# Kernel optimization log

Measured on AMD Instinct MI355X. Metric: run time of the kernel, lower is better.

## Reference

```python
import jax, jax.numpy as jnp
import numpy as np
from jax import lax

B, H, W, CIN = 4, 64, 64, 1024
CMID = 512
NA = 9  # 3 sizes * 3 ratios
PRE_NMS, POST_NMS, IOU_THR = 6000, 300, 0.7  # eval-mode caps (training=False)


def setup_inputs() -> dict:
    key = jax.random.key(0)
    ks = jax.random.split(key, 4)
    feats = jax.random.normal(ks[0], (B, H, W, CIN), jnp.float32)
    # anchors: normalized ccwh (cx, cy, w, h) on a stride-16 grid of a 1024px image
    stride, img = 16.0, 1024.0
    cx = (jnp.arange(W, dtype=jnp.float32) + 0.5) * stride / img
    cy = (jnp.arange(H, dtype=jnp.float32) + 0.5) * stride / img
    sizes = jnp.array([64.0, 128.0, 256.0])
    ratios = jnp.array([0.5, 1.0, 2.0])
    ws = (sizes[:, None] * jnp.sqrt(ratios)[None, :]).reshape(-1) / img  # [9]
    hs = (sizes[:, None] / jnp.sqrt(ratios)[None, :]).reshape(-1) / img  # [9]
    cyg, cxg = jnp.meshgrid(cy, cx, indexing='ij')  # [H,W]
    ancs = jnp.stack([
        jnp.broadcast_to(cxg[:, :, None], (H, W, NA)),
        jnp.broadcast_to(cyg[:, :, None], (H, W, NA)),
        jnp.broadcast_to(ws[None, None, :], (H, W, NA)),
        jnp.broadcast_to(hs[None, None, :], (H, W, NA)),
    ], axis=-1)
    ancs = jnp.broadcast_to(ancs[None], (B, H, W, NA, 4)).astype(jnp.float32)
    ancs_valid = jnp.ones((B, H, W, NA), jnp.float32)
    w_bneck = jax.random.normal(ks[1], (CIN, CMID), jnp.float32) * 0.01
    b_bneck = jnp.zeros((CMID,), jnp.float32)
    w_cls = jax.random.normal(ks[2], (CMID, NA), jnp.float32) * 0.01
    b_cls = jnp.zeros((NA,), jnp.float32)
    w_reg = jax.random.normal(ks[3], (CMID, NA * 4), jnp.float32) * 0.01
    b_reg = jnp.zeros((NA * 4,), jnp.float32)
    return dict(feats=feats, ancs=ancs, ancs_valid=ancs_valid,
                w_bneck=w_bneck, b_bneck=b_bneck, w_cls=w_cls, b_cls=b_cls,
                w_reg=w_reg, b_reg=b_reg)


def _nms(boxes, max_out, thr):
    # boxes [N,4] xyxy, sorted by score descending. Greedy NMS via lax.scan.
    x1, y1, x2, y2 = boxes[:, 0], boxes[:, 1], boxes[:, 2], boxes[:, 3]
    areas = (x2 - x1) * (y2 - y1)

    def step(valid, _):
        idx = jnp.argmax(valid)  # first still-valid box = highest score
        has = valid[idx]
        b = boxes[idx]
        a = areas[idx]
        iw = jnp.maximum(jnp.minimum(b[2], x2) - jnp.maximum(b[0], x1), 0.0)
        ih = jnp.maximum(jnp.minimum(b[3], y2) - jnp.maximum(b[1], y1), 0.0)
        inter = iw * ih
        union = a + areas - inter
        iou = jnp.where(union > 0, inter / union, 0.0)
        keep = valid & (iou <= thr)
        keep = keep.at[idx].set(False)
        return jnp.where(has, keep, valid), jnp.where(has, idx, -1)

    _, sel = lax.scan(step, jnp.ones(boxes.shape[0], bool), None, length=max_out)
    return sel  # [max_out] selected indices, -1 = no more boxes


def _forward(feats, ancs, w_bneck, b_bneck, w_cls, b_cls, w_reg, b_reg):
    h = jax.nn.relu(jnp.einsum('bhwc,cm->bhwm', feats, w_bneck) + b_bneck)
    cls_pred = jax.nn.sigmoid(jnp.einsum('bhwm,mo->bhwo', h, w_cls) + b_cls)
    reg_pred = (jnp.einsum('bhwm,mo->bhwo', h, w_reg) + b_reg).reshape(B, H, W, NA, 4)
    cls_f = cls_pred.reshape(-1)
    reg_f = reg_pred.reshape(-1, 4)
    anc_f = ancs.reshape(-1, 4)
    # apply_offsets in ccwh: cx += tx*w, cy += ty*h, w *= exp(tw), h *= exp(th)
    cx = anc_f[:, 0] + reg_f[:, 0] * anc_f[:, 2]
    cy = anc_f[:, 1] + reg_f[:, 1] * anc_f[:, 3]
    ww = anc_f[:, 2] * jnp.exp(reg_f[:, 2])
    hh = anc_f[:, 3] * jnp.exp(reg_f[:, 3])
    # ccwh -> xyxy, clip to [0,1]
    boxes = jnp.stack([cx - ww / 2, cy - hh / 2, cx + ww / 2, cy + hh / 2], axis=-1)
    boxes = jnp.clip(boxes, 0.0, 1.0)
    order = jnp.argsort(-cls_f)[:PRE_NMS]
    boxes = boxes[order]
    sel = _nms(boxes, POST_NMS, IOU_THR)
    # pad unselected slots with zeros (TF returns a variable-length tensor)
    proposals = jnp.where(sel[:, None] >= 0, boxes[jnp.clip(sel, 0)], 0.0)
    return cls_pred, reg_pred, proposals


def reference(feats, ancs, ancs_valid, w_bneck, b_bneck, w_cls, b_cls, w_reg, b_reg):
    # ancs_valid is reshaped but never used in the original extract_proposals
    return _forward(feats, ancs, w_bneck, b_bneck, w_cls, b_cls, w_reg, b_reg)
```

## Files before the change

### kernel.cpp

```cpp
#include <hip/hip_runtime.h>
#include <cstdint>
#include <cstddef>

#define P_TOT    16384
#define CIN      1024
#define CMID     512
#define NA       9
#define NANC     147456
#define PRE_NMS  6000
#define POST_NMS 300
#define IOU_THR  0.7f
#define NWORDS   94
#define NHCOPY   8

#define CLS_OFF  0
#define REG_OFF  147456
#define PROP_OFF 737280

#define WS_H        0u
#define WS_MASK     0u
#define WS_HISTN    33554432u
#define WS_BOXES    36700160u
#define WS_HIST     39059456u
#define WS_WCOMB    39059456u
#define WS_META     39321600u
#define WS_COLL     39321856u
#define WS_SBOX     39387392u
#define CAP_COLL    8192

__device__ __forceinline__ int imin(int a, int b) { return a < b ? a : b; }

__device__ __forceinline__ void gld_lds16f(const float* g, float* l) {
    __builtin_amdgcn_global_load_lds(
        (const __attribute__((address_space(1))) void*)g,
        (__attribute__((address_space(3))) void*)l,
        16, 0, 0);
}

__global__ __launch_bounds__(256)
__attribute__((amdgpu_waves_per_eu(1, 2)))
void gemm1_kernel(
    const float* __restrict__ A, const float* __restrict__ Bw,
    const float* __restrict__ bias, float* __restrict__ C)
{
    __shared__ float As[2][32][132];
    __shared__ float Bs[2][32][128];

    const int t  = threadIdx.x;
    const int m0 = blockIdx.x * 128;
    const int n0 = blockIdx.y * 128;
    const int tx = t & 15;
    const int ty = t >> 4;

    const int ar0 = t >> 1;
    const int ac0 = (t & 1) * 16;

    const float* asrc = A + (size_t)(m0 + ar0) * CIN + ac0;
    const float* bsrc = Bw + (size_t)(t >> 5) * CMID + n0 + (t & 31) * 4;
    float* bflat = &Bs[0][0][0];

    float4 c0a{0,0,0,0}, c0b{0,0,0,0}, c1a{0,0,0,0}, c1b{0,0,0,0};
    float4 c2a{0,0,0,0}, c2b{0,0,0,0}, c3a{0,0,0,0}, c3b{0,0,0,0};
    float4 c4a{0,0,0,0}, c4b{0,0,0,0}, c5a{0,0,0,0}, c5b{0,0,0,0};
    float4 c6a{0,0,0,0}, c6b{0,0,0,0}, c7a{0,0,0,0}, c7b{0,0,0,0};

#define ASTAGE(buf, v0, v1, v2, v3) { \
    As[buf][ac0 +  0][ar0] = v0.x; As[buf][ac0 +  1][ar0] = v0.y; \
    As[buf][ac0 +  2][ar0] = v0.z; As[buf][ac0 +  3][ar0] = v0.w; \
    As[buf][ac0 +  4][ar0] = v1.x; As[buf][ac0 +  5][ar0] = v1.y; \
    As[buf][ac0 +  6][ar0] = v1.z; As[buf][ac0 +  7][ar0] = v1.w; \
    As[buf][ac0 +  8][ar0] = v2.x; As[buf][ac0 +  9][ar0] = v2.y; \
    As[buf][ac0 + 10][ar0] = v2.z; As[buf][ac0 + 11][ar0] = v2.w; \
    As[buf][ac0 + 12][ar0] = v3.x; As[buf][ac0 + 13][ar0] = v3.y; \
    As[buf][ac0 + 14][ar0] = v3.z; As[buf][ac0 + 15][ar0] = v3.w; }

    {
        gld_lds16f(bsrc,                      bflat +    0 + t * 4);
        gld_lds16f(bsrc + (size_t) 8 * CMID,  bflat + 1024 + t * 4);
        gld_lds16f(bsrc + (size_t)16 * CMID,  bflat + 2048 + t * 4);
        gld_lds16f(bsrc + (size_t)24 * CMID,  bflat + 3072 + t * 4);
        float4 av0 = *(const float4*)(asrc + 0);
        float4 av1 = *(const float4*)(asrc + 4);
        float4 av2 = *(const float4*)(asrc + 8);
        float4 av3 = *(const float4*)(asrc + 12);
        ASTAGE(0, av0, av1, av2, av3)
    }
    __syncthreads();

#define FMA4(acc, s, b) { acc.x += (s)*(b).x; acc.y += (s)*(b).y; \
                          acc.z += (s)*(b).z; acc.w += (s)*(b).w; }

    for (int kt = 0; kt < 32; ++kt) {
        const int cur = kt & 1, nxt = cur ^ 1;
        float4 av0, av1, av2, av3;
        if (kt < 31) {
            const int k0 = (kt + 1) * 32;
            float* bd = bflat + nxt * 4096 + t * 4;
            gld_lds16f(bsrc + (size_t)(k0     ) * CMID, bd);
            gld_lds16f(bsrc + (size_t)(k0 +  8) * CMID, bd + 1024);
            gld_lds16f(bsrc + (size_t)(k0 + 16) * CMID, bd + 2048);
            gld_lds16f(bsrc + (size_t)(k0 + 24) * CMID, bd + 3072);
            av0 = *(const float4*)(asrc + k0);
            av1 = *(const float4*)(asrc + k0 + 4);
            av2 = *(const float4*)(asrc + k0 + 8);
            av3 = *(const float4*)(asrc + k0 + 12);
        }
#pragma unroll 2
        for (int kk = 0; kk < 32; ++kk) {
            float4 a0 = *(const float4*)&As[cur][kk][ty * 4];
            float4 a1 = *(const float4*)&As[cur][kk][64 + ty * 4];
            float4 b0 = *(const float4*)&Bs[cur][kk][tx * 4];
            float4 b1 = *(const float4*)&Bs[cur][kk][64 + tx * 4];
            FMA4(c0a, a0.x, b0) FMA4(c0b, a0.x, b1)
            FMA4(c1a, a0.y, b0) FMA4(c1b, a0.y, b1)
            FMA4(c2a, a0.z, b0) FMA4(c2b, a0.z, b1)
            FMA4(c3a, a0.w, b0) FMA4(c3b, a0.w, b1)
            FMA4(c4a, a1.x, b0) FMA4(c4b, a1.x, b1)
            FMA4(c5a, a1.y, b0) FMA4(c5b, a1.y, b1)
            FMA4(c6a, a1.z, b0) FMA4(c6b, a1.z, b1)
            FMA4(c7a, a1.w, b0) FMA4(c7b, a1.w, b1)
        }
        if (kt < 31) {
            ASTAGE(nxt, av0, av1, av2, av3)
        }
        __syncthreads();
    }
#undef FMA4
#undef ASTAGE

    const float4 bias0 = *(const float4*)(bias + n0 + tx * 4);
    const float4 bias1 = *(const float4*)(bias + n0 + 64 + tx * 4);
#define STROW(row, ca, cb) { \
    float4 o; \
    o.x = fmaxf(ca.x + bias0.x, 0.f); o.y = fmaxf(ca.y + bias0.y, 0.f); \
    o.z = fmaxf(ca.z + bias0.z, 0.f); o.w = fmaxf(ca.w + bias0.w, 0.f); \
    *(float4*)(C + (size_t)(row) * CMID + n0 + tx * 4) = o; \
    o.x = fmaxf(cb.x + bias1.x, 0.f); o.y = fmaxf(cb.y + bias1.y, 0.f); \
    o.z = fmaxf(cb.z + bias1.z, 0.f); o.w = fmaxf(cb.w + bias1.w, 0.f); \
    *(float4*)(C + (size_t)(row) * CMID + n0 + 64 + tx * 4) = o; }

    const int mr = m0 + ty * 4;
    STROW(mr + 0, c0a, c0b)   STROW(mr + 1, c1a, c1b)
    STROW(mr + 2, c2a, c2b)   STROW(mr + 3, c3a, c3b)
    STROW(mr + 64, c4a, c4b)  STROW(mr + 65, c5a, c5b)
    STROW(mr + 66, c6a, c6b)  STROW(mr + 67, c7a, c7b)
#undef STROW
}

__global__ __launch_bounds__(256) void wprep_kernel(
    const float* __restrict__ wcls, const float* __restrict__ wreg,
    float* __restrict__ wcomb)
{
    int i = blockIdx.x * 256 + threadIdx.x;
    int k = i / 48, o = i - k * 48;
    float v = 0.f;
    if (o < 9)       v = wcls[k * 9 + o];
    else if (o < 45) v = wreg[k * 36 + (o - 9)];
    wcomb[i] = v;
}

__global__ __launch_bounds__(256) void gemm2_kernel(
    const float* __restrict__ h, const float* __restrict__ wcomb,
    const float* __restrict__ bcls, const float* __restrict__ breg,
    const float4* __restrict__ ancs, float* __restrict__ out,
    float4* __restrict__ boxes, unsigned int* __restrict__ histN)
{
    __shared__ float hS[32][33];
    __shared__ float wS[32][48];
    __shared__ float lt[32][49];

    const int t  = threadIdx.x;
    const int p0 = blockIdx.x * 32;
    const int px = t & 31;
    const int og = t >> 5;

    const int hr = t >> 3;
    const int hc = (t & 7) * 4;

    float acc[6] = {};

    for (int kt = 0; kt < 16; ++kt) {
        const int k0 = kt * 32;
        {
            const float* hp = h + (size_t)(p0 + hr) * CMID + k0 + hc;
            float4 v0 = *(const float4*)(hp);
            hS[hr][hc + 0] = v0.x; hS[hr][hc + 1] = v0.y;
            hS[hr][hc + 2] = v0.z; hS[hr][hc + 3] = v0.w;
        }
        {
            int idx = t;
            if (idx < 384) {
                int kk = idx / 12, o4 = (idx - kk * 12) * 4;
                *(float4*)&wS[kk][o4] = *(const float4*)&wcomb[(size_t)(k0 + kk) * 48 + o4];
            }
            idx = t + 256;
            if (idx < 384) {
                int kk = idx / 12, o4 = (idx - kk * 12) * 4;
                *(float4*)&wS[kk][o4] = *(const float4*)&wcomb[(size_t)(k0 + kk) * 48 + o4];
            }
        }
        __syncthreads();
#pragma unroll 4
        for (int kk = 0; kk < 32; ++kk) {
            float hv = hS[px][kk];
            float2 w0 = *(const float2*)&wS[kk][og * 6];
            float2 w1 = *(const float2*)&wS[kk][og * 6 + 2];
            float2 w2 = *(const float2*)&wS[kk][og * 6 + 4];
            acc[0] += hv * w0.x; acc[1] += hv * w0.y;
            acc[2] += hv * w1.x; acc[3] += hv * w1.y;
            acc[4] += hv * w2.x; acc[5] += hv * w2.y;
        }
        __syncthreads();
    }

#pragma unroll
    for (int c = 0; c < 6; ++c) {
        int o = og * 6 + c;
        float v = 0.f;
        if (o < 45) {
            float bv = (o < 9) ? bcls[o] : breg[o - 9];
            v = acc[c] + bv;
        }
        lt[px][o] = v;
    }
    __syncthreads();

#pragma unroll
    for (int rr = 0; rr < 2; ++rr) {
        int a_lin = t + rr * 256;
        if (a_lin < 288) {
            int px_l = a_lin / 9;
            int a    = a_lin - px_l * 9;
            int i    = (p0 + px_l) * 9 + a;

            float lg = lt[px_l][a];
            float score = 1.f / (1.f + expf(-lg));
            out[CLS_OFF + i] = score;

            float r0 = lt[px_l][9 + a * 4 + 0];
            float r1 = lt[px_l][9 + a * 4 + 1];
            float r2 = lt[px_l][9 + a * 4 + 2];
            float r3 = lt[px_l][9 + a * 4 + 3];
            float4 rg; rg.x = r0; rg.y = r1; rg.z = r2; rg.w = r3;
            *(float4*)(out + REG_OFF + (size_t)i * 4) = rg;

            float4 an = ancs[i];
            float cx = an.x + r0 * an.z;
            float cy = an.y + r1 * an.w;
            float ww = an.z * expf(r2);
            float hh = an.w * expf(r3);
            float4 bb;
            bb.x = fminf(fmaxf(cx - ww * 0.5f, 0.f), 1.f);
            bb.y = fminf(fmaxf(cy - hh * 0.5f, 0.f), 1.f);
            bb.z = fminf(fmaxf(cx + ww * 0.5f, 0.f), 1.f);
            bb.w = fminf(fmaxf(cy + hh * 0.5f, 0.f), 1.f);
            boxes[i] = bb;

            unsigned int sb = __float_as_uint(score);
            atomicAdd(&histN[(unsigned)(blockIdx.x & (NHCOPY - 1)) * 65536u + (sb >> 16)], 1u);
        }
    }
}

__global__ __launch_bounds__(256) void hreduce_kernel(
    const unsigned int* __restrict__ histN, unsigned int* __restrict__ hist)
{
    int b = blockIdx.x * 256 + threadIdx.x;
    unsigned int s = 0;
#pragma unroll
    for (int c = 0; c < NHCOPY; ++c) s += histN[(unsigned)c * 65536u + b];
    hist[b] = s;
}

__global__ __launch_bounds__(256) void scan_kernel(
    const unsigned int* __restrict__ hist, unsigned int* __restrict__ meta)
{
    __shared__ unsigned int sums[256];
    __shared__ unsigned int sc[256];
    __shared__ unsigned int sc2[256];
    __shared__ int cstar;
    __shared__ unsigned int saShared;
    __shared__ int tbin;

    int t = threadIdx.x;
    if (t == 0) tbin = -1;

    unsigned int s = 0;
    int base = t << 8;
    for (int b = 0; b < 256; b += 4) {
        uint4 v = *(const uint4*)(hist + base + b);
        s += v.x + v.y + v.z + v.w;
    }
    sums[t] = s;
    __syncthreads();

    sc[t] = sums[255 - t];
    __syncthreads();
    for (int off = 1; off < 256; off <<= 1) {
        unsigned int v = sc[t];
        unsigned int add = (t >= off) ? sc[t - off] : 0u;
        __syncthreads();
        sc[t] = v + add;
        __syncthreads();
    }
    {
        unsigned int sa = (t == 255) ? 0u : sc[254 - t];
        if (sa < PRE_NMS && sa + sums[t] >= PRE_NMS) { cstar = t; saShared = sa; }
    }
    __syncthreads();

    int c = cstar;
    unsigned int SA = saShared;
    sc2[t] = hist[c * 256 + 255 - t];
    __syncthreads();
    for (int off = 1; off < 256; off <<= 1) {
        unsigned int v = sc2[t];
        unsigned int add = (t >= off) ? sc2[t - off] : 0u;
        __syncthreads();
        sc2[t] = v + add;
        __syncthreads();
    }
    {
        unsigned int si = sc2[255 - t];
        int cand = (SA + si >= PRE_NMS) ? t : -1;
        atomicMax(&tbin, cand);
    }
    __syncthreads();
    if (t == 0) meta[1] = (unsigned int)(c * 256 + tbin);
}

__global__ __launch_bounds__(256) void collect_kernel(
    const float* __restrict__ scores, const unsigned int* __restrict__ meta,
    unsigned long long* __restrict__ coll, unsigned int* __restrict__ cnt)
{
    int i = blockIdx.x * 256 + threadIdx.x;
    unsigned int T = meta[1];
    unsigned int sb = __float_as_uint(scores[i]);
    if ((sb >> 16) >= T) {
        unsigned int pos = atomicAdd(cnt, 1u);
        if (pos < CAP_COLL)
            coll[pos] = ((unsigned long long)sb << 32) |
                        (unsigned long long)(0xFFFFFFFFu - (unsigned int)i);
    }
}

__global__ __launch_bounds__(256) void rank_kernel(
    const unsigned long long* __restrict__ coll,
    const unsigned int* __restrict__ cnt,
    const float4* __restrict__ boxes, float4* __restrict__ sboxes)
{
    const int t = threadIdx.x;
    const int lane = t & 63;
    const int gwave = blockIdx.x * 4 + (t >> 6);
    unsigned int n = cnt[0];
    if (n > CAP_COLL) n = CAP_COLL;
    if (gwave * 16 >= (int)n) return;

    unsigned long long me[16];
    int rank[16];
#pragma unroll
    for (int i = 0; i < 16; ++i) {
        int mi = gwave * 16 + i;
        me[i] = (mi < (int)n) ? coll[mi] : ~0ULL;
        rank[i] = 0;
    }

    for (int j = 0; j < CAP_COLL; j += 64) {
        unsigned long long k = ((unsigned)(j + lane) < n) ? coll[j + lane] : 0ULL;
#pragma unroll
        for (int i = 0; i < 16; ++i)
            rank[i] += (int)__popcll(__ballot(k > me[i]));
    }

#pragma unroll
    for (int i = 0; i < 16; ++i) {
        int mi = gwave * 16 + i;
        if (mi < (int)n && rank[i] < PRE_NMS && lane == i) {
            unsigned int idx = 0xFFFFFFFFu - (unsigned int)(me[i] & 0xFFFFFFFFULL);
            if (idx > NANC - 1) idx = NANC - 1;
            sboxes[rank[i]] = boxes[idx];
        }
    }
}

__global__ __launch_bounds__(64) void nmsmat_kernel(
    const float4* __restrict__ sboxes, unsigned long long* __restrict__ mask)
{
    const int rb = blockIdx.x, cb = blockIdx.y;
    if (cb < rb) return;
    __shared__ float cx1[64], cy1[64], cx2[64], cy2[64], car[64];

    const int t = threadIdx.x;
    const int c = cb * 64 + t;
    float4 b = (c < PRE_NMS) ? sboxes[c] : make_float4(0.f, 0.f, 0.f, 0.f);
    cx1[t] = b.x; cy1[t] = b.y; cx2[t] = b.z; cy2[t] = b.w;
    car[t] = (b.z - b.x) * (b.w - b.y);
    __syncthreads();

    const int r = rb * 64 + t;
    if (r >= PRE_NMS) return;
    const float4 rbx = sboxes[r];
    const float ra = (rbx.z - rbx.x) * (rbx.w - rbx.y);

    unsigned long long w = 0ULL;
#pragma unroll 8
    for (int i = 0; i < 64; ++i) {
        int j = cb * 64 + i;
        float iw = fmaxf(fminf(rbx.z, cx2[i]) - fmaxf(rbx.x, cx1[i]), 0.f);
        float ih = fmaxf(fminf(rbx.w, cy2[i]) - fmaxf(rbx.y, cy1[i]), 0.f);
        float inter = iw * ih;
        float uni = ra + car[i] - inter;
        float iou = (uni > 0.f) ? (inter / uni) : 0.f;
        if (iou > IOU_THR && j > r) w |= (1ULL << i);
    }
    mask[(size_t)r * NWORDS + cb] = w;
}

__global__ __launch_bounds__(64) void nmsresolve_kernel(
    const float4* __restrict__ sboxes,
    const unsigned long long* __restrict__ mask,
    float* __restrict__ prop)
{
    const int t = threadIdx.x;
    for (int j = t; j < POST_NMS * 4; j += 64) prop[j] = 0.f;

    const int w0 = 2 * t, w1 = 2 * t + 1;
    unsigned long long v0 = 0ULL, v1 = 0ULL;
    if (w0 < 93) v0 = ~0ULL; else if (w0 == 93) v0 = (1ULL << 48) - 1ULL;
    if (w1 < 93) v1 = ~0ULL; else if (w1 == 93) v1 = (1ULL << 48) - 1ULL;

    int cnt = 0;
    while (cnt < POST_NMS) {
        int c = 0x7fffffff;
        if (v0) c = (w0 << 6) + __builtin_ctzll(v0);
        else if (v1) c = (w1 << 6) + __builtin_ctzll(v1);
        unsigned long long bal = __ballot((v0 | v1) != 0ULL);
        if (!bal) break;
        int F = __builtin_ctzll(bal);
        int g = __shfl(c, F, 64);
        const int wg = g >> 6, bg = g & 63;

        if (t == 0) {
            float4 bb = sboxes[g];
            *(float4*)(prop + cnt * 4) = bb;
        }
        unsigned long long mx = 0ULL, my = 0ULL;
        if (t < 47) {
            const ulonglong2* row2 = (const ulonglong2*)(mask + (size_t)g * NWORDS);
            ulonglong2 mm = row2[t];
            mx = mm.x; my = mm.y;
        }
        unsigned long long m0 = (w0 >= wg) ? mx : 0ULL;
        unsigned long long m1 = (w1 >= wg) ? my : 0ULL;
        v0 &= ~m0; v1 &= ~m1;
        if (w0 == wg) v0 &= ~(1ULL << bg);
        if (w1 == wg) v1 &= ~(1ULL << bg);
        ++cnt;
    }
}

extern "C" void kernel_launch(void* const* d_in, const int* in_sizes, int n_in,
                              void* d_out, int out_size, void* d_ws, size_t ws_size,
                              hipStream_t stream)
{
    const float*  feats   = (const float*)d_in[0];
    const float4* ancs    = (const float4*)d_in[1];
    const float*  w_bneck = (const float*)d_in[3];
    const float*  b_bneck = (const float*)d_in[4];
    const float*  w_cls   = (const float*)d_in[5];
    const float*  b_cls   = (const float*)d_in[6];
    const float*  w_reg   = (const float*)d_in[7];
    const float*  b_reg   = (const float*)d_in[8];

    float* out = (float*)d_out;
    char*  ws  = (char*)d_ws;
    float*              h      = (float*)(ws + WS_H);
    float4*             boxes  = (float4*)(ws + WS_BOXES);
    unsigned int*       histN  = (unsigned int*)(ws + WS_HISTN);
    unsigned int*       hist   = (unsigned int*)(ws + WS_HIST);
    float*              wcomb  = (float*)(ws + WS_WCOMB);
    unsigned int*       meta   = (unsigned int*)(ws + WS_META);
    unsigned long long* coll   = (unsigned long long*)(ws + WS_COLL);
    float4*             sboxes = (float4*)(ws + WS_SBOX);
    unsigned long long* mask   = (unsigned long long*)(ws + WS_MASK);

    hipMemsetAsync(ws + WS_META, 0, 256, stream);
    hipMemsetAsync(ws + WS_HISTN, 0, (size_t)NHCOPY * 65536 * 4, stream);

    wprep_kernel<<<96, 256, 0, stream>>>(w_cls, w_reg, wcomb);
    gemm1_kernel<<<dim3(128, 4), 256, 0, stream>>>(feats, w_bneck, b_bneck, h);
    gemm2_kernel<<<512, 256, 0, stream>>>(h, wcomb, b_cls, b_reg,
                                          ancs, out, boxes, histN);
    hreduce_kernel<<<256, 256, 0, stream>>>(histN, hist);
    scan_kernel<<<1, 256, 0, stream>>>(hist, meta);
    collect_kernel<<<576, 256, 0, stream>>>(out, meta, coll, &meta[0]);
    rank_kernel<<<128, 256, 0, stream>>>(coll, meta, boxes, sboxes);
    nmsmat_kernel<<<dim3(94, 94), 64, 0, stream>>>(sboxes, mask);
    nmsresolve_kernel<<<1, 64, 0, stream>>>(sboxes, mask, out + PROP_OFF);
}
```

Baseline: 653.8 us.

## Fold memsets, weight prep and histogram reduce into neighbouring kernels; halve gemm1 K-tile

Removes the two memsets, the wprep kernel and the hreduce kernel by zeroing the histogram and meta inside gemm1, gathering the cls/reg weights directly in gemm2, and summing the histogram copies inside scan. It also halves the histogram copy count, changes gemm1 to 16-wide K tiles with a different A staging pattern, and adds extra waves in nmsresolve that stream the NMS mask to warm the cache. The goal is to cut launch overhead and small kernels. In exchange the single-block scan does more serial reads, there is more atomic contention on fewer histogram copies, and gemm1 now hits twice as many barriers.

```diff
diff --git a/kernel.cpp b/kernel.cpp
--- a/kernel.cpp
+++ b/kernel.cpp
@@ -11,7 +11,7 @@
 #define POST_NMS 300
 #define IOU_THR  0.7f
 #define NWORDS   94
-#define NHCOPY   8
+#define NHCOPY   4
 
 #define CLS_OFF  0
 #define REG_OFF  147456
@@ -21,8 +21,6 @@
 #define WS_MASK     0u
 #define WS_HISTN    33554432u
 #define WS_BOXES    36700160u
-#define WS_HIST     39059456u
-#define WS_WCOMB    39059456u
 #define WS_META     39321600u
 #define WS_COLL     39321856u
 #define WS_SBOX     39387392u
@@ -41,72 +39,67 @@
 __attribute__((amdgpu_waves_per_eu(1, 2)))
 void gemm1_kernel(
     const float* __restrict__ A, const float* __restrict__ Bw,
-    const float* __restrict__ bias, float* __restrict__ C)
-{
-    __shared__ float As[2][32][132];
-    __shared__ float Bs[2][32][128];
+    const float* __restrict__ bias, float* __restrict__ C,
+    unsigned int* __restrict__ histN, unsigned int* __restrict__ meta)
+{
+    __shared__ float As[2][16][132];
+    __shared__ float Bs[2][16][128];
 
     const int t  = threadIdx.x;
+
+    {
+        const int fb = (int)blockIdx.x * 4 + (int)blockIdx.y;
+        if (t < 128) {
+            uint4* hz = (uint4*)histN;
+            hz[fb * 128 + t] = make_uint4(0u, 0u, 0u, 0u);
+        }
+        if (fb == 0 && t < 64) meta[t] = 0u;
+    }
+
     const int m0 = blockIdx.x * 128;
     const int n0 = blockIdx.y * 128;
     const int tx = t & 15;
     const int ty = t >> 4;
 
-    const int ar0 = t >> 1;
-    const int ac0 = (t & 1) * 16;
-
-    const float* asrc = A + (size_t)(m0 + ar0) * CIN + ac0;
-    const float* bsrc = Bw + (size_t)(t >> 5) * CMID + n0 + (t & 31) * 4;
-    float* bflat = &Bs[0][0][0];
+    const int ar0 = t >> 2;
+    const int ac0 = (t & 3) * 4;
+
+    const float* asrc0 = A + (size_t)(m0 + ar0) * CIN + ac0;
+    const float* asrc1 = asrc0 + (size_t)64 * CIN;
+    const float* bsrc  = Bw + (size_t)(t >> 5) * CMID + n0 + (t & 31) * 4;
+    float* bdst0 = &Bs[0][0][0] + t * 4;
+    float* bdst1 = &Bs[1][0][0] + t * 4;
 
     float4 c0a{0,0,0,0}, c0b{0,0,0,0}, c1a{0,0,0,0}, c1b{0,0,0,0};
     float4 c2a{0,0,0,0}, c2b{0,0,0,0}, c3a{0,0,0,0}, c3b{0,0,0,0};
     float4 c4a{0,0,0,0}, c4b{0,0,0,0}, c5a{0,0,0,0}, c5b{0,0,0,0};
     float4 c6a{0,0,0,0}, c6b{0,0,0,0}, c7a{0,0,0,0}, c7b{0,0,0,0};
 
-#define ASTAGE(buf, v0, v1, v2, v3) { \
-    As[buf][ac0 +  0][ar0] = v0.x; As[buf][ac0 +  1][ar0] = v0.y; \
-    As[buf][ac0 +  2][ar0] = v0.z; As[buf][ac0 +  3][ar0] = v0.w; \
-    As[buf][ac0 +  4][ar0] = v1.x; As[buf][ac0 +  5][ar0] = v1.y; \
-    As[buf][ac0 +  6][ar0] = v1.z; As[buf][ac0 +  7][ar0] = v1.w; \
-    As[buf][ac0 +  8][ar0] = v2.x; As[buf][ac0 +  9][ar0] = v2.y; \
-    As[buf][ac0 + 10][ar0] = v2.z; As[buf][ac0 + 11][ar0] = v2.w; \
-    As[buf][ac0 + 12][ar0] = v3.x; As[buf][ac0 + 13][ar0] = v3.y; \
-    As[buf][ac0 + 14][ar0] = v3.z; As[buf][ac0 + 15][ar0] = v3.w; }
-
-    {
-        gld_lds16f(bsrc,                      bflat +    0 + t * 4);
-        gld_lds16f(bsrc + (size_t) 8 * CMID,  bflat + 1024 + t * 4);
-        gld_lds16f(bsrc + (size_t)16 * CMID,  bflat + 2048 + t * 4);
-        gld_lds16f(bsrc + (size_t)24 * CMID,  bflat + 3072 + t * 4);
-        float4 av0 = *(const float4*)(asrc + 0);
-        float4 av1 = *(const float4*)(asrc + 4);
-        float4 av2 = *(const float4*)(asrc + 8);
-        float4 av3 = *(const float4*)(asrc + 12);
-        ASTAGE(0, av0, av1, av2, av3)
-    }
+    gld_lds16f(bsrc, bdst0);
+    gld_lds16f(bsrc + 8 * CMID, bdst0 + 1024);
+    float4 pa0 = *(const float4*)(asrc0);
+    float4 pa1 = *(const float4*)(asrc1);
+    As[0][ac0 + 0][ar0] = pa0.x; As[0][ac0 + 1][ar0] = pa0.y;
+    As[0][ac0 + 2][ar0] = pa0.z; As[0][ac0 + 3][ar0] = pa0.w;
+    As[0][ac0 + 0][ar0 + 64] = pa1.x; As[0][ac0 + 1][ar0 + 64] = pa1.y;
+    As[0][ac0 + 2][ar0 + 64] = pa1.z; As[0][ac0 + 3][ar0 + 64] = pa1.w;
     __syncthreads();
 
 #define FMA4(acc, s, b) { acc.x += (s)*(b).x; acc.y += (s)*(b).y; \
                           acc.z += (s)*(b).z; acc.w += (s)*(b).w; }
 
-    for (int kt = 0; kt < 32; ++kt) {
+    for (int kt = 0; kt < 64; ++kt) {
         const int cur = kt & 1, nxt = cur ^ 1;
-        float4 av0, av1, av2, av3;
-        if (kt < 31) {
-            const int k0 = (kt + 1) * 32;
-            float* bd = bflat + nxt * 4096 + t * 4;
-            gld_lds16f(bsrc + (size_t)(k0     ) * CMID, bd);
-            gld_lds16f(bsrc + (size_t)(k0 +  8) * CMID, bd + 1024);
-            gld_lds16f(bsrc + (size_t)(k0 + 16) * CMID, bd + 2048);
-            gld_lds16f(bsrc + (size_t)(k0 + 24) * CMID, bd + 3072);
-            av0 = *(const float4*)(asrc + k0);
-            av1 = *(const float4*)(asrc + k0 + 4);
-            av2 = *(const float4*)(asrc + k0 + 8);
-            av3 = *(const float4*)(asrc + k0 + 12);
+        if (kt < 63) {
+            const int k0 = (kt + 1) * 16;
+            float* bd = nxt ? bdst1 : bdst0;
+            gld_lds16f(bsrc + (size_t)k0 * CMID, bd);
+            gld_lds16f(bsrc + (size_t)(k0 + 8) * CMID, bd + 1024);
+            pa0 = *(const float4*)(asrc0 + k0);
+            pa1 = *(const float4*)(asrc1 + k0);
         }
 #pragma unroll 2
-        for (int kk = 0; kk < 32; ++kk) {
+        for (int kk = 0; kk < 16; ++kk) {
             float4 a0 = *(const float4*)&As[cur][kk][ty * 4];
             float4 a1 = *(const float4*)&As[cur][kk][64 + ty * 4];
             float4 b0 = *(const float4*)&Bs[cur][kk][tx * 4];
@@ -120,13 +113,15 @@
             FMA4(c6a, a1.z, b0) FMA4(c6b, a1.z, b1)
             FMA4(c7a, a1.w, b0) FMA4(c7b, a1.w, b1)
         }
-        if (kt < 31) {
-            ASTAGE(nxt, av0, av1, av2, av3)
+        if (kt < 63) {
+            As[nxt][ac0 + 0][ar0] = pa0.x; As[nxt][ac0 + 1][ar0] = pa0.y;
+            As[nxt][ac0 + 2][ar0] = pa0.z; As[nxt][ac0 + 3][ar0] = pa0.w;
+            As[nxt][ac0 + 0][ar0 + 64] = pa1.x; As[nxt][ac0 + 1][ar0 + 64] = pa1.y;
+            As[nxt][ac0 + 2][ar0 + 64] = pa1.z; As[nxt][ac0 + 3][ar0 + 64] = pa1.w;
         }
         __syncthreads();
     }
 #undef FMA4
-#undef ASTAGE
 
     const float4 bias0 = *(const float4*)(bias + n0 + tx * 4);
     const float4 bias1 = *(const float4*)(bias + n0 + 64 + tx * 4);
@@ -147,20 +142,9 @@
 #undef STROW
 }
 
-__global__ __launch_bounds__(256) void wprep_kernel(
+__global__ __launch_bounds__(256) void gemm2_kernel(
+    const float* __restrict__ h,
     const float* __restrict__ wcls, const float* __restrict__ wreg,
-    float* __restrict__ wcomb)
-{
-    int i = blockIdx.x * 256 + threadIdx.x;
-    int k = i / 48, o = i - k * 48;
-    float v = 0.f;
-    if (o < 9)       v = wcls[k * 9 + o];
-    else if (o < 45) v = wreg[k * 36 + (o - 9)];
-    wcomb[i] = v;
-}
-
-__global__ __launch_bounds__(256) void gemm2_kernel(
-    const float* __restrict__ h, const float* __restrict__ wcomb,
     const float* __restrict__ bcls, const float* __restrict__ breg,
     const float4* __restrict__ ancs, float* __restrict__ out,
     float4* __restrict__ boxes, unsigned int* __restrict__ histN)
@@ -188,15 +172,13 @@
             hS[hr][hc + 2] = v0.z; hS[hr][hc + 3] = v0.w;
         }
         {
-            int idx = t;
-            if (idx < 384) {
-                int kk = idx / 12, o4 = (idx - kk * 12) * 4;
-                *(float4*)&wS[kk][o4] = *(const float4*)&wcomb[(size_t)(k0 + kk) * 48 + o4];
-            }
-            idx = t + 256;
-            if (idx < 384) {
-                int kk = idx / 12, o4 = (idx - kk * 12) * 4;
-                *(float4*)&wS[kk][o4] = *(const float4*)&wcomb[(size_t)(k0 + kk) * 48 + o4];
+#pragma unroll
+            for (int s = t; s < 1536; s += 256) {
+                int o = s >> 5, kk = s & 31;
+                float v = 0.f;
+                if (o < 9)       v = wcls[(size_t)(k0 + kk) * 9 + o];
+                else if (o < 45) v = wreg[(size_t)(k0 + kk) * 36 + (o - 9)];
+                wS[kk][o] = v;
             }
         }
         __syncthreads();
@@ -262,18 +244,8 @@
     }
 }
 
-__global__ __launch_bounds__(256) void hreduce_kernel(
-    const unsigned int* __restrict__ histN, unsigned int* __restrict__ hist)
-{
-    int b = blockIdx.x * 256 + threadIdx.x;
-    unsigned int s = 0;
-#pragma unroll
-    for (int c = 0; c < NHCOPY; ++c) s += histN[(unsigned)c * 65536u + b];
-    hist[b] = s;
-}
-
 __global__ __launch_bounds__(256) void scan_kernel(
-    const unsigned int* __restrict__ hist, unsigned int* __restrict__ meta)
+    const unsigned int* __restrict__ histN, unsigned int* __restrict__ meta)
 {
     __shared__ unsigned int sums[256];
     __shared__ unsigned int sc[256];
@@ -287,9 +259,12 @@
 
     unsigned int s = 0;
     int base = t << 8;
-    for (int b = 0; b < 256; b += 4) {
-        uint4 v = *(const uint4*)(hist + base + b);
-        s += v.x + v.y + v.z + v.w;
+    for (int c = 0; c < NHCOPY; ++c) {
+        const uint4* hp = (const uint4*)(histN + (size_t)c * 65536u + base);
+        for (int b = 0; b < 64; ++b) {
+            uint4 v = hp[b];
+            s += v.x + v.y + v.z + v.w;
+        }
     }
     sums[t] = s;
     __syncthreads();
@@ -311,7 +286,13 @@
 
     int c = cstar;
     unsigned int SA = saShared;
-    sc2[t] = hist[c * 256 + 255 - t];
+    {
+        unsigned int bs = 0;
+        int bin = c * 256 + 255 - t;
+        for (int cc = 0; cc < NHCOPY; ++cc)
+            bs += histN[(size_t)cc * 65536u + bin];
+        sc2[t] = bs;
+    }
     __syncthreads();
     for (int off = 1; off < 256; off <<= 1) {
         unsigned int v = sc2[t];
@@ -416,12 +397,25 @@
     mask[(size_t)r * NWORDS + cb] = w;
 }
 
-__global__ __launch_bounds__(64) void nmsresolve_kernel(
+__global__ __launch_bounds__(256) void nmsresolve_kernel(
     const float4* __restrict__ sboxes,
     const unsigned long long* __restrict__ mask,
     float* __restrict__ prop)
 {
     const int t = threadIdx.x;
+
+    if (t >= 64) {
+        const int pid = t - 64;
+        const ulonglong2* m2 = (const ulonglong2*)mask;
+        unsigned long long acc = 0;
+        for (int i = pid; i < 282000; i += 192) {
+            ulonglong2 v = m2[i];
+            acc ^= v.x ^ v.y;
+        }
+        asm volatile("" :: "v"(acc));
+        return;
+    }
+
     for (int j = t; j < POST_NMS * 4; j += 64) prop[j] = 0.f;
 
     const int w0 = 2 * t, w1 = 2 * t + 1;
@@ -477,24 +471,18 @@
     float*              h      = (float*)(ws + WS_H);
     float4*             boxes  = (float4*)(ws + WS_BOXES);
     unsigned int*       histN  = (unsigned int*)(ws + WS_HISTN);
-    unsigned int*       hist   = (unsigned int*)(ws + WS_HIST);
-    float*              wcomb  = (float*)(ws + WS_WCOMB);
     unsigned int*       meta   = (unsigned int*)(ws + WS_META);
     unsigned long long* coll   = (unsigned long long*)(ws + WS_COLL);
     float4*             sboxes = (float4*)(ws + WS_SBOX);
     unsigned long long* mask   = (unsigned long long*)(ws + WS_MASK);
 
-    hipMemsetAsync(ws + WS_META, 0, 256, stream);
-    hipMemsetAsync(ws + WS_HISTN, 0, (size_t)NHCOPY * 65536 * 4, stream);
-
-    wprep_kernel<<<96, 256, 0, stream>>>(w_cls, w_reg, wcomb);
-    gemm1_kernel<<<dim3(128, 4), 256, 0, stream>>>(feats, w_bneck, b_bneck, h);
-    gemm2_kernel<<<512, 256, 0, stream>>>(h, wcomb, b_cls, b_reg,
+    gemm1_kernel<<<dim3(128, 4), 256, 0, stream>>>(feats, w_bneck, b_bneck, h,
+                                                   histN, meta);
+    gemm2_kernel<<<512, 256, 0, stream>>>(h, w_cls, w_reg, b_cls, b_reg,
                                           ancs, out, boxes, histN);
-    hreduce_kernel<<<256, 256, 0, stream>>>(histN, hist);
-    scan_kernel<<<1, 256, 0, stream>>>(hist, meta);
+    scan_kernel<<<1, 256, 0, stream>>>(histN, meta);
     collect_kernel<<<576, 256, 0, stream>>>(out, meta, coll, &meta[0]);
     rank_kernel<<<128, 256, 0, stream>>>(coll, meta, boxes, sboxes);
     nmsmat_kernel<<<dim3(94, 94), 64, 0, stream>>>(sboxes, mask);
-    nmsresolve_kernel<<<1, 64, 0, stream>>>(sboxes, mask, out + PROP_OFF);
-}
+    nmsresolve_kernel<<<1, 256, 0, stream>>>(sboxes, mask, out + PROP_OFF);
+}
```

Result: slower. 963.5 us (+47.4%).
